# Performance work log

Measured on AMD Instinct MI355X. Metric: run time of the kernel, lower is better.

Reference implementation:

```python
import jax, jax.numpy as jnp
import numpy as np

B, N, D = 64, 512, 128  # graphs per batch, max nodes per graph, hidden_dim


def setup_inputs() -> dict:
    key = jax.random.key(0)
    ks = jax.random.split(key, 9)
    h1 = jax.random.normal(ks[0], (B, N, D), jnp.float32)
    h2 = jax.random.normal(ks[1], (B, N, D), jnp.float32)
    s = 1.0 / np.sqrt(D)
    Wk = jax.random.normal(ks[2], (D, D), jnp.float32) * s
    bk = jax.random.normal(ks[3], (D,), jnp.float32) * s
    Wq = jax.random.normal(ks[4], (D, D), jnp.float32) * s
    bq = jax.random.normal(ks[5], (D,), jnp.float32) * s
    t = jnp.asarray(np.sqrt(1.0 / D), jnp.float32)  # self.t = sqrt(1/hidden_dim)
    len1 = jax.random.randint(ks[6], (B,), 1, N + 1, jnp.int32)
    len2 = jax.random.randint(ks[7], (B,), 1, N + 1, jnp.int32)
    return {"h1": h1, "h2": h2, "Wk": Wk, "bk": bk, "Wq": Wq, "bq": bq,
            "t": t, "len1": len1, "len2": len2}


def reference(h1, h2, Wk, bk, Wq, bq, t, len1, len2):
    # valid-node masks for the ragged (padded) graphs
    pos = jnp.arange(N)
    m1 = pos[None, :] < len1[:, None]  # [B, N]
    m2 = pos[None, :] < len2[:, None]  # [B, N]

    # k = Linear(h), q = Linear(h)  (torch Linear: x @ W.T + b)
    k1 = jnp.einsum('bnd,ed->bne', h1, Wk) + bk
    k2 = jnp.einsum('bnd,ed->bne', h2, Wk) + bk
    q1 = jnp.einsum('bnd,ed->bne', h1, Wq) + bq
    q2 = jnp.einsum('bnd,ed->bne', h2, Wq) + bq

    NEG = jnp.asarray(-1e9, h1.dtype)

    # g1 nodes attend over g2 nodes; note values == keys (k2)
    s1 = jnp.einsum('bnd,bmd->bnm', q1, k2) * t           # [B, N1, N2]
    s1 = jnp.where(m2[:, None, :], s1, NEG)
    a1 = jax.nn.softmax(s1, axis=-1)
    o1 = jnp.einsum('bnm,bmd->bnd', a1, k2) * m1[:, :, None]

    # g2 nodes attend over g1 nodes; values == k1
    s2 = jnp.einsum('bnd,bmd->bnm', q2, k1) * t           # [B, N2, N1]
    s2 = jnp.where(m1[:, None, :], s2, NEG)
    a2 = jax.nn.softmax(s2, axis=-1)
    o2 = jnp.einsum('bnm,bmd->bnd', a2, k1) * m2[:, :, None]

    return o1, o2
```

## Files before the change

kernel.cpp:

```cpp
#include <hip/hip_runtime.h>

typedef __attribute__((ext_vector_type(8))) short bf16x8;
typedef __attribute__((ext_vector_type(4))) short s16x4;
typedef __attribute__((ext_vector_type(4))) float f32x4;
typedef __attribute__((ext_vector_type(4))) int   i32x4;

#define MFMA16 __builtin_amdgcn_mfma_f32_16x16x32_bf16

#define B_ 64
#define N_ 512
#define D_ 128

__device__ __forceinline__ unsigned short f2bf(float f) {
  unsigned u = __builtin_bit_cast(unsigned, f);
  u += 0x7fffu + ((u >> 16) & 1u);
  return (unsigned short)(u >> 16);
}
__device__ __forceinline__ int packbf2(float lo, float hi) {
  return (int)((unsigned)f2bf(lo) | ((unsigned)f2bf(hi) << 16));
}

__global__ void prep_w(const float* __restrict__ Wk, const float* __restrict__ Wq,
                       const float* __restrict__ bq, const float* __restrict__ tptr,
                       short* __restrict__ wkb, short* __restrict__ wqb,
                       float* __restrict__ bqs) {
  const float sc = tptr[0] * 1.4426950408889634f;
  int i = blockIdx.x * 256 + threadIdx.x;
  if (i < D_ * D_) { wkb[i] = (short)f2bf(Wk[i]); wqb[i] = (short)f2bf(Wq[i] * sc); }
  if (i < D_) bqs[i] = bq[i] * sc;
}

__global__ __launch_bounds__(256, 2) void proj_kernel(
    const float* __restrict__ h1, const float* __restrict__ h2,
    const short* __restrict__ wkb, const short* __restrict__ wqb,
    const float* __restrict__ bk, const float* __restrict__ bqs,
    short* __restrict__ k1, short* __restrict__ k2,
    short* __restrict__ q1, short* __restrict__ q2,
    short* __restrict__ v1t, short* __restrict__ v2t) {
  const int wave = threadIdx.x >> 6, lane = threadIdx.x & 63;
  const int c = lane & 15, g = lane >> 4;
  const int rw = blockIdx.x * 128 + wave * 32;
  const int inp = rw >> 15;
  const int loc = rw & 32767;
  const int b = loc >> 9, n0 = loc & 511;
  const float* __restrict__ h = inp ? h2 : h1;
  short* __restrict__ kout = inp ? k2 : k1;
  short* __restrict__ qout = inp ? q2 : q1;
  short* __restrict__ vt   = inp ? v2t : v1t;

  bf16x8 xf[2][4];
#pragma unroll
  for (int mt = 0; mt < 2; ++mt) {
    const float* hr = h + (long)(loc + mt * 16 + c) * D_;
#pragma unroll
    for (int kk = 0; kk < 4; ++kk) {
      f32x4 lo = *(const f32x4*)(hr + kk * 32 + g * 8);
      f32x4 hi = *(const f32x4*)(hr + kk * 32 + g * 8 + 4);
      bf16x8 v;
      v[0] = (short)f2bf(lo[0]); v[1] = (short)f2bf(lo[1]);
      v[2] = (short)f2bf(lo[2]); v[3] = (short)f2bf(lo[3]);
      v[4] = (short)f2bf(hi[0]); v[5] = (short)f2bf(hi[1]);
      v[6] = (short)f2bf(hi[2]); v[7] = (short)f2bf(hi[3]);
      xf[mt][kk] = v;
    }
  }

#pragma unroll
  for (int et = 0; et < 8; ++et) {
    bf16x8 wkf[4], wqf[4];
    const short* wkr = wkb + (et * 16 + c) * D_;
    const short* wqr = wqb + (et * 16 + c) * D_;
#pragma unroll
    for (int kk = 0; kk < 4; ++kk) {
      wkf[kk] = *(const bf16x8*)(wkr + kk * 32 + g * 8);
      wqf[kk] = *(const bf16x8*)(wqr + kk * 32 + g * 8);
    }
    f32x4 ak[2], aq[2], at[2];
#pragma unroll
    for (int mt = 0; mt < 2; ++mt) {
      ak[mt] = (f32x4){0.f, 0.f, 0.f, 0.f};
      aq[mt] = (f32x4){0.f, 0.f, 0.f, 0.f};
      at[mt] = (f32x4){0.f, 0.f, 0.f, 0.f};
    }
#pragma unroll
    for (int kk = 0; kk < 4; ++kk) {
#pragma unroll
      for (int mt = 0; mt < 2; ++mt) {
        ak[mt] = MFMA16(wkf[kk], xf[mt][kk], ak[mt], 0, 0, 0);
        aq[mt] = MFMA16(wqf[kk], xf[mt][kk], aq[mt], 0, 0, 0);
        at[mt] = MFMA16(xf[mt][kk], wkf[kk], at[mt], 0, 0, 0);
      }
    }
    f32x4 bkv = *(const f32x4*)(bk + et * 16 + g * 4);
    f32x4 bqv = *(const f32x4*)(bqs + et * 16 + g * 4);
    float bks = bk[et * 16 + c];
#pragma unroll
    for (int mt = 0; mt < 2; ++mt) {
      s16x4 pk, pq, pt;
#pragma unroll
      for (int j = 0; j < 4; ++j) {
        pk[j] = (short)f2bf(ak[mt][j] + bkv[j]);
        pq[j] = (short)f2bf(aq[mt][j] + bqv[j]);
        pt[j] = (short)f2bf(at[mt][j] + bks);
      }
      long row = (long)(loc + mt * 16 + c);
      *(s16x4*)(kout + row * D_ + et * 16 + g * 4) = pk;
      *(s16x4*)(qout + row * D_ + et * 16 + g * 4) = pq;
      *(s16x4*)(vt + (long)b * 65536 + (n0 >> 5) * 4096 +
                (et * 16 + c) * 32 + mt * 16 + g * 4) = pt;
    }
  }
}

__global__ __launch_bounds__(64, 2) void attn_kernel(
    const short* __restrict__ k1, const short* __restrict__ k2,
    const short* __restrict__ q1, const short* __restrict__ q2,
    const short* __restrict__ v1t, const short* __restrict__ v2t,
    const int* __restrict__ len1, const int* __restrict__ len2,
    float* __restrict__ out) {
  const int lane = threadIdx.x;
  const int c = lane & 15, g = lane >> 4;
  const int bid = blockIdx.x;
  const int bd = (bid & 7) | ((bid >> 7) << 3);
  const int qt = (bid >> 3) & 15;
  const int dir = bd >> 6, b = bd & 63;
  const short* __restrict__ qp = dir ? q2 : q1;
  const short* __restrict__ kp = dir ? k1 : k2;
  const short* __restrict__ vp = dir ? v1t : v2t;
  const int lk = dir ? len1[b] : len2[b];
  const int lq = dir ? len2[b] : len1[b];
  float* __restrict__ o = out + (long)dir * B_ * N_ * D_;
  const int q0 = qt * 32;

  if (q0 >= lq) {
    f32x4 z = (f32x4){0.f, 0.f, 0.f, 0.f};
    f32x4* op = (f32x4*)(o + ((long)(b * N_ + q0)) * D_);
#pragma unroll
    for (int i = 0; i < 16; ++i) op[i * 64 + lane] = z;
    return;
  }

  const char* kbase = (const char*)(kp + (long)b * N_ * D_);
  const short* vbase = vp + (long)b * 65536;

  bf16x8 qf[2][4];
#pragma unroll
  for (int t = 0; t < 2; ++t) {
    const short* qrow = qp + ((long)(b * N_ + q0 + t * 16 + c)) * D_;
#pragma unroll
    for (int kk = 0; kk < 4; ++kk) qf[t][kk] = *(const bf16x8*)(qrow + kk * 32 + g * 8);
  }

  f32x4 oacc[2][8];
#pragma unroll
  for (int t = 0; t < 2; ++t)
#pragma unroll
    for (int dt = 0; dt < 8; ++dt) oacc[t][dt] = (f32x4){0.f, 0.f, 0.f, 0.f};
  float lp[2] = {0.f, 0.f};

  const int srcA = c + ((g & 1) << 5);
  const int srcB = srcA + 16;
  const bool lowhalf = (g < 2);
  const int nch = (lk + 31) >> 5;

  auto loadk = [&](bf16x8 (&kf)[2][4], int ch) {
#pragma unroll
    for (int tl = 0; tl < 2; ++tl) {
      const char* base = kbase + (ch * 32 + tl * 16 + c) * 256;
#pragma unroll
      for (int kk = 0; kk < 4; ++kk)
        kf[tl][kk] = *(const bf16x8*)(base + kk * 64 + g * 16);
    }
  };

  auto body = [&](bf16x8 (&kfc)[2][4], bf16x8 (&kfn)[2][4], int ch) {
    const short* vchunk = vbase + ch * 4096;
    bf16x8 vt[8];
#pragma unroll
    for (int dt = 0; dt < 8; ++dt)
      vt[dt] = *(const bf16x8*)(vchunk + (dt * 16 + c) * 32 + g * 8);
    __builtin_amdgcn_sched_barrier(0);

    f32x4 sv[2][2];
#pragma unroll
    for (int tl = 0; tl < 2; ++tl) {
      f32x4 a0 = (f32x4){0.f, 0.f, 0.f, 0.f};
      f32x4 a1 = (f32x4){0.f, 0.f, 0.f, 0.f};
#pragma unroll
      for (int kk = 0; kk < 4; ++kk) {
        a0 = MFMA16(kfc[tl][kk], qf[0][kk], a0, 0, 0, 0);
        a1 = MFMA16(kfc[tl][kk], qf[1][kk], a1, 0, 0, 0);
      }
      sv[0][tl] = a0; sv[1][tl] = a1;
    }

    if (ch + 1 < nch) loadk(kfn, ch + 1);
    __builtin_amdgcn_sched_barrier(0);

    const bool lastch = (ch == nch - 1);
    bf16x8 pf[2];
#pragma unroll
    for (int t = 0; t < 2; ++t) {
      if (lastch) {
#pragma unroll
        for (int tl = 0; tl < 2; ++tl) {
          const int node = ch * 32 + tl * 16 + g * 4;
#pragma unroll
          for (int j = 0; j < 4; ++j)
            if (node + j >= lk) sv[t][tl][j] = -1e9f;
        }
      }
      float sum = 0.f;
#pragma unroll
      for (int tl = 0; tl < 2; ++tl)
#pragma unroll
        for (int j = 0; j < 4; ++j) {
          float p = exp2f(sv[t][tl][j]);
          sv[t][tl][j] = p;
          sum += p;
        }
      lp[t] += sum;

      int a0 = packbf2(sv[t][0][0], sv[t][0][1]);
      int a1 = packbf2(sv[t][0][2], sv[t][0][3]);
      int b0 = packbf2(sv[t][1][0], sv[t][1][1]);
      int b1 = packbf2(sv[t][1][2], sv[t][1][3]);
      int xa0 = __shfl(a0, srcA), xb0 = __shfl(b0, srcA);
      int xa1 = __shfl(a1, srcA), xb1 = __shfl(b1, srcA);
      int ya0 = __shfl(a0, srcB), yb0 = __shfl(b0, srcB);
      int ya1 = __shfl(a1, srcB), yb1 = __shfl(b1, srcB);
      i32x4 ui;
      ui[0] = lowhalf ? xa0 : xb0;
      ui[1] = lowhalf ? xa1 : xb1;
      ui[2] = lowhalf ? ya0 : yb0;
      ui[3] = lowhalf ? ya1 : yb1;
      pf[t] = __builtin_bit_cast(bf16x8, ui);
    }

#pragma unroll
    for (int dt = 0; dt < 8; ++dt) {
      oacc[0][dt] = MFMA16(vt[dt], pf[0], oacc[0][dt], 0, 0, 0);
      oacc[1][dt] = MFMA16(vt[dt], pf[1], oacc[1][dt], 0, 0, 0);
    }
  };

  bf16x8 kfA[2][4], kfB[2][4];
  loadk(kfA, 0);
  int ch = 0;
  while (true) {
    body(kfA, kfB, ch);
    if (++ch >= nch) break;
    body(kfB, kfA, ch);
    if (++ch >= nch) break;
  }

#pragma unroll
  for (int t = 0; t < 2; ++t) {
    lp[t] += __shfl_xor(lp[t], 16);
    lp[t] += __shfl_xor(lp[t], 32);
    const int qg = q0 + t * 16 + c;
    const bool valid = qg < lq;
    const float rinv = 1.0f / lp[t];
    float* orow = o + ((long)(b * N_ + qg)) * D_;
#pragma unroll
    for (int dt = 0; dt < 8; ++dt) {
      f32x4 vo;
#pragma unroll
      for (int j = 0; j < 4; ++j) vo[j] = valid ? oacc[t][dt][j] * rinv : 0.0f;
      *(f32x4*)(orow + dt * 16 + g * 4) = vo;
    }
  }
}

extern "C" void kernel_launch(void* const* d_in, const int* in_sizes, int n_in,
                              void* d_out, int out_size, void* d_ws, size_t ws_size,
                              hipStream_t stream) {
  const float* h1 = (const float*)d_in[0];
  const float* h2 = (const float*)d_in[1];
  const float* Wk = (const float*)d_in[2];
  const float* bk = (const float*)d_in[3];
  const float* Wq = (const float*)d_in[4];
  const float* bq = (const float*)d_in[5];
  const float* t  = (const float*)d_in[6];
  const int* len1 = (const int*)d_in[7];
  const int* len2 = (const int*)d_in[8];

  char* ws = (char*)d_ws;
  const size_t SZ = (size_t)B_ * N_ * D_ * 2;
  short* k1  = (short*)(ws + 0 * SZ);
  short* k2  = (short*)(ws + 1 * SZ);
  short* q1  = (short*)(ws + 2 * SZ);
  short* q2  = (short*)(ws + 3 * SZ);
  short* v1t = (short*)(ws + 4 * SZ);
  short* v2t = (short*)(ws + 5 * SZ);
  short* wkb = (short*)(ws + 6 * SZ);
  short* wqb = (short*)(ws + 6 * SZ + D_ * D_ * 2);
  float* bqs = (float*)(ws + 6 * SZ + 2 * D_ * D_ * 2);

  prep_w<<<64, 256, 0, stream>>>(Wk, Wq, bq, t, wkb, wqb, bqs);
  proj_kernel<<<512, 256, 0, stream>>>(h1, h2, wkb, wqb, bk, bqs,
                                       k1, k2, q1, q2, v1t, v2t);
  attn_kernel<<<2048, 64, 0, stream>>>(k1, k2, q1, q2, v1t, v2t,
                                       len1, len2, (float*)d_out);
}
```

Baseline: 78.50 us.

## Split key chunks across two waves per query tile and reduce via LDS

Each attention block now runs two waves that process alternating key/value chunks for the same 32-query tile. Each wave keeps its own partial output accumulator and softmax denominator, and the two halves are combined through shared memory after a block barrier, with each wave writing half of the output columns. The aim is to shorten the serial chunk loop per tile and raise the number of waves per CU. In exchange it adds LDS traffic, a __syncthreads, and duplicated Q-fragment loads per wave. It appears to rely on a fixed softmax offset (no running max), so the partial sums combine directly.

```diff
diff --git a/kernel.cpp b/kernel.cpp
--- a/kernel.cpp
+++ b/kernel.cpp
@@ -112,13 +112,16 @@
   }
 }
 
-__global__ __launch_bounds__(64, 2) void attn_kernel(
+__global__ __launch_bounds__(128, 4) void attn_kernel(
     const short* __restrict__ k1, const short* __restrict__ k2,
     const short* __restrict__ q1, const short* __restrict__ q2,
     const short* __restrict__ v1t, const short* __restrict__ v2t,
     const int* __restrict__ len1, const int* __restrict__ len2,
     float* __restrict__ out) {
-  const int lane = threadIdx.x;
+  __shared__ f32x4 lds_o[2][2][4][64];
+  __shared__ float lds_l[2][2][64];
+  const int tid = threadIdx.x;
+  const int wave = tid >> 6, lane = tid & 63;
   const int c = lane & 15, g = lane >> 4;
   const int bid = blockIdx.x;
   const int bd = (bid & 7) | ((bid >> 7) << 3);
@@ -136,7 +139,7 @@
     f32x4 z = (f32x4){0.f, 0.f, 0.f, 0.f};
     f32x4* op = (f32x4*)(o + ((long)(b * N_ + q0)) * D_);
 #pragma unroll
-    for (int i = 0; i < 16; ++i) op[i * 64 + lane] = z;
+    for (int i = 0; i < 8; ++i) op[i * 128 + tid] = z;
     return;
   }
 
@@ -194,7 +197,7 @@
       sv[0][tl] = a0; sv[1][tl] = a1;
     }
 
-    if (ch + 1 < nch) loadk(kfn, ch + 1);
+    if (ch + 2 < nch) loadk(kfn, ch + 2);
     __builtin_amdgcn_sched_barrier(0);
 
     const bool lastch = (ch == nch - 1);
@@ -244,29 +247,49 @@
     }
   };
 
-  bf16x8 kfA[2][4], kfB[2][4];
-  loadk(kfA, 0);
-  int ch = 0;
-  while (true) {
-    body(kfA, kfB, ch);
-    if (++ch >= nch) break;
-    body(kfB, kfA, ch);
-    if (++ch >= nch) break;
-  }
-
+  {
+    bf16x8 kfA[2][4], kfB[2][4];
+    int ch = wave;
+    if (ch < nch) {
+      loadk(kfA, ch);
+      while (true) {
+        body(kfA, kfB, ch);
+        ch += 2;
+        if (ch >= nch) break;
+        body(kfB, kfA, ch);
+        ch += 2;
+        if (ch >= nch) break;
+      }
+    }
+  }
+
+  const int ow = wave ^ 1;
 #pragma unroll
   for (int t = 0; t < 2; ++t) {
-    lp[t] += __shfl_xor(lp[t], 16);
-    lp[t] += __shfl_xor(lp[t], 32);
+#pragma unroll
+    for (int i = 0; i < 4; ++i)
+      lds_o[wave][t][i][lane] = oacc[t][ow * 4 + i];
+    lds_l[wave][t][lane] = lp[t];
+  }
+  __syncthreads();
+
+#pragma unroll
+  for (int t = 0; t < 2; ++t) {
+    float lsum = lp[t] + lds_l[ow][t][lane];
+    lsum += __shfl_xor(lsum, 16);
+    lsum += __shfl_xor(lsum, 32);
+    const float rinv = 1.0f / lsum;
     const int qg = q0 + t * 16 + c;
     const bool valid = qg < lq;
-    const float rinv = 1.0f / lp[t];
     float* orow = o + ((long)(b * N_ + qg)) * D_;
 #pragma unroll
-    for (int dt = 0; dt < 8; ++dt) {
+    for (int i = 0; i < 4; ++i) {
+      const int dt = wave * 4 + i;
+      f32x4 mine = oacc[t][dt];
+      f32x4 oth = lds_o[ow][t][i][lane];
       f32x4 vo;
 #pragma unroll
-      for (int j = 0; j < 4; ++j) vo[j] = valid ? oacc[t][dt][j] * rinv : 0.0f;
+      for (int j = 0; j < 4; ++j) vo[j] = valid ? (mine[j] + oth[j]) * rinv : 0.0f;
       *(f32x4*)(orow + dt * 16 + g * 4) = vo;
     }
   }
@@ -300,6 +323,6 @@
   prep_w<<<64, 256, 0, stream>>>(Wk, Wq, bq, t, wkb, wqb, bqs);
   proj_kernel<<<512, 256, 0, stream>>>(h1, h2, wkb, wqb, bk, bqs,
                                        k1, k2, q1, q2, v1t, v2t);
-  attn_kernel<<<2048, 64, 0, stream>>>(k1, k2, q1, q2, v1t, v2t,
-                                       len1, len2, (float*)d_out);
-}
+  attn_kernel<<<2048, 128, 0, stream>>>(k1, k2, q1, q2, v1t, v2t,
+                                        len1, len2, (float*)d_out);
+}
```

New measurement: 205.0 us. +161.2%, slower.
